# Kernel optimization log

Measured on AMD Instinct MI355X. Metric: run time of the kernel, lower is better.

## Reference

```python
import jax, jax.numpy as jnp
import numpy as np

N = 100000      # nodes
E = 800000      # edges (avg degree 8)
F_IN = 512      # num_features
H = 256         # 2 * embedding_size
D_OUT = 128     # embedding_size


def setup_inputs() -> dict:
    key = jax.random.key(0)
    ks = jax.random.split(key, 5)
    x = jax.random.normal(ks[0], (N, F_IN), dtype=jnp.float32)
    edge_index = jax.random.randint(ks[1], (2, E), 0, N, dtype=jnp.int64)
    W1 = jax.random.normal(ks[2], (F_IN, H), dtype=jnp.float32) * (1.0 / np.sqrt(F_IN))
    b1 = jnp.zeros((H,), dtype=jnp.float32)
    W2 = jax.random.normal(ks[3], (H, D_OUT), dtype=jnp.float32) * (1.0 / np.sqrt(H))
    b2 = jnp.zeros((D_OUT,), dtype=jnp.float32)
    return {"x": x, "edge_index": edge_index, "W1": W1, "b1": b1, "W2": W2, "b2": b2}


def _gcn_conv(x, edge_index, W, b):
    # PyG GCNConv: add self-loops, symmetric deg^-1/2 normalization,
    # linear transform, scatter-add aggregation at destination nodes.
    n = x.shape[0]
    loop = jnp.arange(n, dtype=edge_index.dtype)
    src = jnp.concatenate([edge_index[0], loop])  # source j
    dst = jnp.concatenate([edge_index[1], loop])  # target i
    h = x @ W                                      # [N, F_out]
    deg = jax.ops.segment_sum(jnp.ones_like(dst, dtype=h.dtype), dst, num_segments=n)
    dinv = jnp.where(deg > 0, jax.lax.rsqrt(deg), 0.0)
    norm = dinv[src] * dinv[dst]                   # [E + N]
    msg = h[src] * norm[:, None]                   # gather + scale
    out = jax.ops.segment_sum(msg, dst, num_segments=n)
    return out + b


def reference(x, edge_index, W1, b1, W2, b2):
    h = jax.nn.relu(_gcn_conv(x, edge_index, W1, b1))
    # F.dropout with training=False is identity (eval mode)
    return _gcn_conv(h, edge_index, W2, b2)
```

## Files before the change

kernel.cpp:

```cpp
#include <hip/hip_runtime.h>


typedef float   f32x4  __attribute__((ext_vector_type(4)));
typedef float   f32x2  __attribute__((ext_vector_type(2)));
typedef __bf16  bf16x8 __attribute__((ext_vector_type(8)));
typedef __bf16  bf16x4 __attribute__((ext_vector_type(4)));
typedef __bf16  bf16x2 __attribute__((ext_vector_type(2)));

#define FIN 512
#define HID 256
#define DOUT 128

__device__ __forceinline__ void gload16(const void* g, void* l) {
    __builtin_amdgcn_global_load_lds((const __attribute__((address_space(1))) void*)g,
                                     (__attribute__((address_space(3))) void*)l, 16, 0, 0);
}

__global__ void k_count(const int* __restrict__ dst, int E, int* __restrict__ cnt) {
    int e = blockIdx.x * 256 + threadIdx.x;
    if (e < E) atomicAdd(&cnt[dst[e]], 1);
}

__global__ void k_scan1(const int* __restrict__ cnt, int* __restrict__ off,
                        int* __restrict__ sums, int n) {
    __shared__ int s[1024];
    int i = blockIdx.x * 1024 + threadIdx.x;
    int v = (i < n) ? cnt[i] : 0;
    s[threadIdx.x] = v;
    __syncthreads();
    for (int d = 1; d < 1024; d <<= 1) {
        int t = (threadIdx.x >= d) ? s[threadIdx.x - d] : 0;
        __syncthreads();
        s[threadIdx.x] += t;
        __syncthreads();
    }
    if (i < n) off[i] = s[threadIdx.x] - v;
    if (threadIdx.x == 1023) sums[blockIdx.x] = s[1023];
}

__global__ void k_scan2(int* __restrict__ sums, int nb) {
    __shared__ int s[128];
    int t = threadIdx.x;
    int v = (t < nb) ? sums[t] : 0;
    s[t] = v;
    __syncthreads();
    for (int d = 1; d < 128; d <<= 1) {
        int u = (t >= d) ? s[t - d] : 0;
        __syncthreads();
        s[t] += u;
        __syncthreads();
    }
    if (t < nb) sums[t] = s[t] - v;
}

__global__ void k_scan_fix(int* __restrict__ off, const int* __restrict__ sums,
                           const int* __restrict__ cnt, float* __restrict__ dinv, int n) {
    int i = blockIdx.x * 256 + threadIdx.x;
    if (i < n) {
        off[i] += sums[i >> 10];
        dinv[i] = rsqrtf((float)(cnt[i] + 1));
    }
}

__global__ void k_fill(const int* __restrict__ src, const int* __restrict__ dst, int E,
                       const int* __restrict__ off, int* __restrict__ cur,
                       int* __restrict__ csr) {
    int e = blockIdx.x * 256 + threadIdx.x;
    if (e < E) {
        int d = dst[e];
        int p = atomicAdd(&cur[d], 1);
        csr[off[d] + p] = src[e];
    }
}

__global__ void k_prep_w(const float* __restrict__ W1, const float* __restrict__ W2,
                         __bf16* __restrict__ W1t, __bf16* __restrict__ W2t) {
    int id = blockIdx.x * 256 + threadIdx.x;
    if (id < FIN * HID) {
        int k = id >> 8, n = id & 255;
        W1t[n * FIN + k] = (__bf16)W1[id];
    }
    int id2 = id - FIN * HID;
    if (id2 >= 0 && id2 < HID * DOUT) {
        int k = id2 >> 7, n = id2 & 127;
        W2t[n * HID + k] = (__bf16)W2[id2];
    }
}

__global__ __launch_bounds__(256, 2) void k_gemm1(
    const float* __restrict__ x, const __bf16* __restrict__ Bt,
    const float* __restrict__ dinv, __bf16* __restrict__ g1, int M) {
    __shared__ __bf16 Albuf[2][128 * 32];
    __shared__ __bf16 Blbuf[2][256 * 32];

    const int tid = threadIdx.x;
    const int l = tid & 63, wid = tid >> 6;
    const int wm = wid & 1, wn = wid >> 1;
    const int r15 = l & 15, hi = l >> 4;
    const long bm = blockIdx.x;

    const int arow = tid >> 1, aseg = tid & 1;
    long ag = bm * 128 + arow;
    if (ag >= M) ag = M - 1;
    const float* aptr = x + ag * (long)FIN + aseg * 16;
    const int aoff = arow * 32 + aseg * 16;

    const int bo0 = wid * 4096;

    f32x4 acc[4][8] = {};

    auto stageB = [&](int kb, int buf) {
#pragma unroll
        for (int i = 0; i < 4; ++i) {
            int ob = bo0 + i * 1024;
            int o = ob + l * 16;
            int n = o >> 6, cb = o & 63;
            const char* src = (const char*)Bt + (long)n * (FIN * 2) + kb * 64 + cb;
            gload16(src, (char*)&Blbuf[buf][0] + ob);
        }
    };

    stageB(0, 0);
    {
        const f32x4* p = (const f32x4*)aptr;
        f32x4 p0 = p[0], p1 = p[1], p2 = p[2], p3 = p[3];
        bf16x8 w0, w1;
#pragma unroll
        for (int j = 0; j < 4; ++j) {
            w0[j] = (__bf16)p0[j]; w0[j + 4] = (__bf16)p1[j];
            w1[j] = (__bf16)p2[j]; w1[j + 4] = (__bf16)p3[j];
        }
        *(bf16x8*)&Albuf[0][aoff] = w0;
        *(bf16x8*)&Albuf[0][aoff + 8] = w1;
    }
    __syncthreads();

    int cur = 0;
    constexpr int NT = FIN / 32;
    for (int kb = 0; kb < NT; ++kb) {
        const int nxt = cur ^ 1;
        const bool pf = (kb + 1 < NT);
        f32x4 p0, p1, p2, p3;
        if (pf) {
            stageB(kb + 1, nxt);
            const f32x4* p = (const f32x4*)(aptr + (kb + 1) * 32);
            p0 = p[0]; p1 = p[1]; p2 = p[2]; p3 = p[3];
        }

        bf16x8 af[4], bfr[8];
#pragma unroll
        for (int m = 0; m < 4; ++m)
            af[m] = *(const bf16x8*)&Albuf[cur][(wm * 64 + m * 16 + r15) * 32 + hi * 8];
#pragma unroll
        for (int n = 0; n < 8; ++n)
            bfr[n] = *(const bf16x8*)&Blbuf[cur][(wn * 128 + n * 16 + r15) * 32 + hi * 8];
#pragma unroll
        for (int m = 0; m < 4; ++m)
#pragma unroll
            for (int n = 0; n < 8; ++n)
                acc[m][n] = __builtin_amdgcn_mfma_f32_16x16x32_bf16(bfr[n], af[m], acc[m][n], 0, 0, 0);

        if (pf) {
            bf16x8 w0, w1;
#pragma unroll
            for (int j = 0; j < 4; ++j) {
                w0[j] = (__bf16)p0[j]; w0[j + 4] = (__bf16)p1[j];
                w1[j] = (__bf16)p2[j]; w1[j + 4] = (__bf16)p3[j];
            }
            *(bf16x8*)&Albuf[nxt][aoff] = w0;
            *(bf16x8*)&Albuf[nxt][aoff + 8] = w1;
        }
        __syncthreads();
        cur = nxt;
    }

#pragma unroll
    for (int m = 0; m < 4; ++m) {
        long rg = bm * 128 + wm * 64 + m * 16 + r15;
        if (rg >= M) continue;
        float di = dinv[rg];
#pragma unroll
        for (int n = 0; n < 8; ++n) {
            bf16x4 o;
            o[0] = (__bf16)(acc[m][n][0] * di);
            o[1] = (__bf16)(acc[m][n][1] * di);
            o[2] = (__bf16)(acc[m][n][2] * di);
            o[3] = (__bf16)(acc[m][n][3] * di);
            int c = wn * 128 + n * 16 + hi * 4;
            *(bf16x4*)(g1 + rg * (long)HID + c) = o;
        }
    }
}

__global__ __launch_bounds__(256, 3) void k_gemm2(
    const __bf16* __restrict__ z1, const __bf16* __restrict__ Bt,
    const float* __restrict__ dinv, __bf16* __restrict__ g2, int M) {
    __shared__ __bf16 Albuf[2][128 * 32];
    __shared__ __bf16 Blbuf[2][128 * 32];

    const int tid = threadIdx.x;
    const int l = tid & 63, wid = tid >> 6;
    const int wm = wid & 1, wn = wid >> 1;
    const int r15 = l & 15, hi = l >> 4;
    const long bm = blockIdx.x;

    f32x4 acc[4][4] = {};

    auto stage = [&](int kb, int buf) {
#pragma unroll
        for (int i = 0; i < 2; ++i) {
            int ob = wid * 2048 + i * 1024;
            int o = ob + l * 16;
            long r = bm * 128 + (o >> 6);
            if (r >= M) r = M - 1;
            const char* src = (const char*)z1 + r * (HID * 2) + kb * 64 + (o & 63);
            gload16(src, (char*)&Albuf[buf][0] + ob);
        }
#pragma unroll
        for (int i = 0; i < 2; ++i) {
            int ob = wid * 2048 + i * 1024;
            int o = ob + l * 16;
            int n = o >> 6;
            const char* src = (const char*)Bt + (long)n * (HID * 2) + kb * 64 + (o & 63);
            gload16(src, (char*)&Blbuf[buf][0] + ob);
        }
    };

    stage(0, 0);
    __syncthreads();

    int cur = 0;
    constexpr int NT = HID / 32;
    for (int kb = 0; kb < NT; ++kb) {
        const int nxt = cur ^ 1;
        if (kb + 1 < NT) stage(kb + 1, nxt);

        bf16x8 af[4], bfr[4];
#pragma unroll
        for (int m = 0; m < 4; ++m)
            af[m] = *(const bf16x8*)&Albuf[cur][(wm * 64 + m * 16 + r15) * 32 + hi * 8];
#pragma unroll
        for (int n = 0; n < 4; ++n)
            bfr[n] = *(const bf16x8*)&Blbuf[cur][(wn * 64 + n * 16 + r15) * 32 + hi * 8];
#pragma unroll
        for (int m = 0; m < 4; ++m)
#pragma unroll
            for (int n = 0; n < 4; ++n)
                acc[m][n] = __builtin_amdgcn_mfma_f32_16x16x32_bf16(bfr[n], af[m], acc[m][n], 0, 0, 0);

        __syncthreads();
        cur = nxt;
    }

#pragma unroll
    for (int m = 0; m < 4; ++m) {
        long rg = bm * 128 + wm * 64 + m * 16 + r15;
        if (rg >= M) continue;
        float di = dinv[rg];
#pragma unroll
        for (int n = 0; n < 4; ++n) {
            bf16x4 o;
            o[0] = (__bf16)(acc[m][n][0] * di);
            o[1] = (__bf16)(acc[m][n][1] * di);
            o[2] = (__bf16)(acc[m][n][2] * di);
            o[3] = (__bf16)(acc[m][n][3] * di);
            int c = wn * 64 + n * 16 + hi * 4;
            *(bf16x4*)(g2 + rg * (long)DOUT + c) = o;
        }
    }
}

__global__ void k_agg1(const __bf16* __restrict__ g1, const int* __restrict__ csr,
                       const int* __restrict__ off, const int* __restrict__ cnt,
                       const float* __restrict__ dinv, const float* __restrict__ b1,
                       __bf16* __restrict__ z1, int n) {
    int node = blockIdx.x * 4 + (threadIdx.x >> 6);
    if (node >= n) return;
    int l = threadIdx.x & 63;
    const __bf16* base = g1 + (size_t)l * 4;
    bf16x4 v = *(const bf16x4*)(base + (size_t)node * HID);
    float a0 = (float)v[0], a1 = (float)v[1], a2 = (float)v[2], a3 = (float)v[3];
    float c0 = 0.f, c1 = 0.f, c2 = 0.f, c3 = 0.f;
    int e = off[node], e0 = e + cnt[node];
    for (; e + 3 < e0; e += 4) {
        int sA = csr[e], sB = csr[e + 1], sC = csr[e + 2], sD = csr[e + 3];
        bf16x4 uA = *(const bf16x4*)(base + (size_t)sA * HID);
        bf16x4 uB = *(const bf16x4*)(base + (size_t)sB * HID);
        bf16x4 uC = *(const bf16x4*)(base + (size_t)sC * HID);
        bf16x4 uD = *(const bf16x4*)(base + (size_t)sD * HID);
        a0 += (float)uA[0] + (float)uC[0]; c0 += (float)uB[0] + (float)uD[0];
        a1 += (float)uA[1] + (float)uC[1]; c1 += (float)uB[1] + (float)uD[1];
        a2 += (float)uA[2] + (float)uC[2]; c2 += (float)uB[2] + (float)uD[2];
        a3 += (float)uA[3] + (float)uC[3]; c3 += (float)uB[3] + (float)uD[3];
    }
    for (; e < e0; ++e) {
        int s = csr[e];
        bf16x4 u = *(const bf16x4*)(base + (size_t)s * HID);
        a0 += (float)u[0]; a1 += (float)u[1]; a2 += (float)u[2]; a3 += (float)u[3];
    }
    float di = dinv[node];
    f32x4 b = *(const f32x4*)(b1 + l * 4);
    bf16x4 o;
    o[0] = (__bf16)fmaxf((a0 + c0) * di + b[0], 0.f);
    o[1] = (__bf16)fmaxf((a1 + c1) * di + b[1], 0.f);
    o[2] = (__bf16)fmaxf((a2 + c2) * di + b[2], 0.f);
    o[3] = (__bf16)fmaxf((a3 + c3) * di + b[3], 0.f);
    *(bf16x4*)(z1 + (size_t)node * HID + l * 4) = o;
}

__global__ void k_agg2(const __bf16* __restrict__ g2, const int* __restrict__ csr,
                       const int* __restrict__ off, const int* __restrict__ cnt,
                       const float* __restrict__ dinv, const float* __restrict__ b2,
                       float* __restrict__ out, int n) {
    int node = blockIdx.x * 4 + (threadIdx.x >> 6);
    if (node >= n) return;
    int l = threadIdx.x & 63;
    const __bf16* base = g2 + (size_t)l * 2;
    bf16x2 v = *(const bf16x2*)(base + (size_t)node * DOUT);
    float a0 = (float)v[0], a1 = (float)v[1];
    float c0 = 0.f, c1 = 0.f;
    int e = off[node], e0 = e + cnt[node];
    for (; e + 3 < e0; e += 4) {
        int sA = csr[e], sB = csr[e + 1], sC = csr[e + 2], sD = csr[e + 3];
        bf16x2 uA = *(const bf16x2*)(base + (size_t)sA * DOUT);
        bf16x2 uB = *(const bf16x2*)(base + (size_t)sB * DOUT);
        bf16x2 uC = *(const bf16x2*)(base + (size_t)sC * DOUT);
        bf16x2 uD = *(const bf16x2*)(base + (size_t)sD * DOUT);
        a0 += (float)uA[0] + (float)uC[0]; c0 += (float)uB[0] + (float)uD[0];
        a1 += (float)uA[1] + (float)uC[1]; c1 += (float)uB[1] + (float)uD[1];
    }
    for (; e < e0; ++e) {
        int s = csr[e];
        bf16x2 u = *(const bf16x2*)(base + (size_t)s * DOUT);
        a0 += (float)u[0]; a1 += (float)u[1];
    }
    float di = dinv[node];
    f32x2 b = *(const f32x2*)(b2 + l * 2);
    f32x2 o;
    o[0] = (a0 + c0) * di + b[0];
    o[1] = (a1 + c1) * di + b[1];
    *(f32x2*)(out + (size_t)node * DOUT + l * 2) = o;
}

extern "C" void kernel_launch(void* const* d_in, const int* in_sizes, int n_in,
                              void* d_out, int out_size, void* d_ws, size_t ws_size,
                              hipStream_t stream) {
    const float* x  = (const float*)d_in[0];
    const int*   ei = (const int*)d_in[1];
    const float* W1 = (const float*)d_in[2];
    const float* b1 = (const float*)d_in[3];
    const float* W2 = (const float*)d_in[4];
    const float* b2 = (const float*)d_in[5];
    float* out = (float*)d_out;

    const int N = in_sizes[0] / FIN;
    const int E = in_sizes[1] / 2;
    const int* srcA = ei;
    const int* dstA = ei + E;

    uint8_t* w = (uint8_t*)d_ws;
    auto take = [&](size_t bytes) { uint8_t* p = w; w += (bytes + 255) & ~(size_t)255; return p; };
    int*    cnt  = (int*)take((size_t)N * 4);
    int*    cur  = (int*)take((size_t)N * 4);
    int*    off  = (int*)take((size_t)N * 4);
    float*  dinv = (float*)take((size_t)N * 4);
    int*    sums = (int*)take(4096);
    int*    csr  = (int*)take((size_t)E * 4);
    __bf16* W1t  = (__bf16*)take((size_t)FIN * HID * 2);
    __bf16* W2t  = (__bf16*)take((size_t)HID * DOUT * 2);
    __bf16* g1   = (__bf16*)take((size_t)N * HID * 2);
    __bf16* z1   = (__bf16*)take((size_t)N * HID * 2);
    __bf16* g2   = (__bf16*)take((size_t)N * DOUT * 2);

    hipMemsetAsync(cnt, 0, (size_t)N * 4, stream);
    hipMemsetAsync(cur, 0, (size_t)N * 4, stream);
    k_count<<<(E + 255) / 256, 256, 0, stream>>>(dstA, E, cnt);
    int nb = (N + 1023) / 1024;
    k_scan1<<<nb, 1024, 0, stream>>>(cnt, off, sums, N);
    k_scan2<<<1, 128, 0, stream>>>(sums, nb);
    k_scan_fix<<<(N + 255) / 256, 256, 0, stream>>>(off, sums, cnt, dinv, N);
    k_fill<<<(E + 255) / 256, 256, 0, stream>>>(srcA, dstA, E, off, cur, csr);

    k_prep_w<<<(FIN * HID + HID * DOUT + 255) / 256, 256, 0, stream>>>(W1, W2, W1t, W2t);

    const int gm = (N + 127) / 128;

    k_gemm1<<<gm, 256, 0, stream>>>(x, W1t, dinv, g1, N);
    k_agg1<<<(N + 3) / 4, 256, 0, stream>>>(g1, csr, off, cnt, dinv, b1, z1, N);
    k_gemm2<<<gm, 256, 0, stream>>>(z1, W2t, dinv, g2, N);
    k_agg2<<<(N + 3) / 4, 256, 0, stream>>>(g2, csr, off, cnt, dinv, b2, out, N);
}
```

Measured before the change: 564.9 us.

## Widen aggregation gathers to half-wave per node and merge prep launches

The aggregation kernels now give each node 32 lanes instead of 64. Each lane loads 16-byte (layer 1) or 8-byte (layer 2) vectors, and the unroll is deeper at 8 edges per iteration, so more gather loads are in flight. The weight conversion is folded into the degree-count kernel, and the two memsets become one contiguous memset. This cuts launch overhead and raises memory-level parallelism in the gather-bound aggregation, at the cost of more registers per thread.

```diff
diff --git a/kernel.cpp b/kernel.cpp
--- a/kernel.cpp
+++ b/kernel.cpp
@@ -2,10 +2,8 @@
 
 
 typedef float   f32x4  __attribute__((ext_vector_type(4)));
-typedef float   f32x2  __attribute__((ext_vector_type(2)));
 typedef __bf16  bf16x8 __attribute__((ext_vector_type(8)));
 typedef __bf16  bf16x4 __attribute__((ext_vector_type(4)));
-typedef __bf16  bf16x2 __attribute__((ext_vector_type(2)));
 
 #define FIN 512
 #define HID 256
@@ -16,9 +14,25 @@
                                      (__attribute__((address_space(3))) void*)l, 16, 0, 0);
 }
 
-__global__ void k_count(const int* __restrict__ dst, int E, int* __restrict__ cnt) {
-    int e = blockIdx.x * 256 + threadIdx.x;
-    if (e < E) atomicAdd(&cnt[dst[e]], 1);
+__global__ void k_count_prep(const int* __restrict__ dst, int E, int* __restrict__ cnt,
+                             const float* __restrict__ W1, const float* __restrict__ W2,
+                             __bf16* __restrict__ W1t, __bf16* __restrict__ W2t,
+                             int nCountBlk) {
+    if (blockIdx.x < nCountBlk) {
+        int e = blockIdx.x * 256 + threadIdx.x;
+        if (e < E) atomicAdd(&cnt[dst[e]], 1);
+    } else {
+        int id = (blockIdx.x - nCountBlk) * 256 + threadIdx.x;
+        if (id < FIN * HID) {
+            int k = id >> 8, n = id & 255;
+            W1t[n * FIN + k] = (__bf16)W1[id];
+        }
+        int id2 = id - FIN * HID;
+        if (id2 >= 0 && id2 < HID * DOUT) {
+            int k = id2 >> 7, n = id2 & 127;
+            W2t[n * HID + k] = (__bf16)W2[id2];
+        }
+    }
 }
 
 __global__ void k_scan1(const int* __restrict__ cnt, int* __restrict__ off,
@@ -70,20 +84,6 @@
         int d = dst[e];
         int p = atomicAdd(&cur[d], 1);
         csr[off[d] + p] = src[e];
-    }
-}
-
-__global__ void k_prep_w(const float* __restrict__ W1, const float* __restrict__ W2,
-                         __bf16* __restrict__ W1t, __bf16* __restrict__ W2t) {
-    int id = blockIdx.x * 256 + threadIdx.x;
-    if (id < FIN * HID) {
-        int k = id >> 8, n = id & 255;
-        W1t[n * FIN + k] = (__bf16)W1[id];
-    }
-    int id2 = id - FIN * HID;
-    if (id2 >= 0 && id2 < HID * DOUT) {
-        int k = id2 >> 7, n = id2 & 127;
-        W2t[n * HID + k] = (__bf16)W2[id2];
     }
 }
 
@@ -274,72 +274,120 @@
                        const int* __restrict__ off, const int* __restrict__ cnt,
                        const float* __restrict__ dinv, const float* __restrict__ b1,
                        __bf16* __restrict__ z1, int n) {
-    int node = blockIdx.x * 4 + (threadIdx.x >> 6);
+    int node = blockIdx.x * 8 + (threadIdx.x >> 5);
     if (node >= n) return;
-    int l = threadIdx.x & 63;
-    const __bf16* base = g1 + (size_t)l * 4;
-    bf16x4 v = *(const bf16x4*)(base + (size_t)node * HID);
-    float a0 = (float)v[0], a1 = (float)v[1], a2 = (float)v[2], a3 = (float)v[3];
-    float c0 = 0.f, c1 = 0.f, c2 = 0.f, c3 = 0.f;
+    int l = threadIdx.x & 31;
+    const __bf16* base = g1 + (size_t)l * 8;
+    float a[8], c[8];
+    {
+        bf16x8 v = *(const bf16x8*)(base + (size_t)node * HID);
+#pragma unroll
+        for (int j = 0; j < 8; ++j) { a[j] = (float)v[j]; c[j] = 0.f; }
+    }
     int e = off[node], e0 = e + cnt[node];
+    for (; e + 7 < e0; e += 8) {
+        int s0 = csr[e], s1 = csr[e + 1], s2 = csr[e + 2], s3 = csr[e + 3];
+        int s4 = csr[e + 4], s5 = csr[e + 5], s6 = csr[e + 6], s7 = csr[e + 7];
+        bf16x8 u0 = *(const bf16x8*)(base + (size_t)s0 * HID);
+        bf16x8 u1 = *(const bf16x8*)(base + (size_t)s1 * HID);
+        bf16x8 u2 = *(const bf16x8*)(base + (size_t)s2 * HID);
+        bf16x8 u3 = *(const bf16x8*)(base + (size_t)s3 * HID);
+        bf16x8 u4 = *(const bf16x8*)(base + (size_t)s4 * HID);
+        bf16x8 u5 = *(const bf16x8*)(base + (size_t)s5 * HID);
+        bf16x8 u6 = *(const bf16x8*)(base + (size_t)s6 * HID);
+        bf16x8 u7 = *(const bf16x8*)(base + (size_t)s7 * HID);
+#pragma unroll
+        for (int j = 0; j < 8; ++j) {
+            a[j] += (float)u0[j] + (float)u2[j] + (float)u4[j] + (float)u6[j];
+            c[j] += (float)u1[j] + (float)u3[j] + (float)u5[j] + (float)u7[j];
+        }
+    }
     for (; e + 3 < e0; e += 4) {
-        int sA = csr[e], sB = csr[e + 1], sC = csr[e + 2], sD = csr[e + 3];
-        bf16x4 uA = *(const bf16x4*)(base + (size_t)sA * HID);
-        bf16x4 uB = *(const bf16x4*)(base + (size_t)sB * HID);
-        bf16x4 uC = *(const bf16x4*)(base + (size_t)sC * HID);
-        bf16x4 uD = *(const bf16x4*)(base + (size_t)sD * HID);
-        a0 += (float)uA[0] + (float)uC[0]; c0 += (float)uB[0] + (float)uD[0];
-        a1 += (float)uA[1] + (float)uC[1]; c1 += (float)uB[1] + (float)uD[1];
-        a2 += (float)uA[2] + (float)uC[2]; c2 += (float)uB[2] + (float)uD[2];
-        a3 += (float)uA[3] + (float)uC[3]; c3 += (float)uB[3] + (float)uD[3];
+        int s0 = csr[e], s1 = csr[e + 1], s2 = csr[e + 2], s3 = csr[e + 3];
+        bf16x8 u0 = *(const bf16x8*)(base + (size_t)s0 * HID);
+        bf16x8 u1 = *(const bf16x8*)(base + (size_t)s1 * HID);
+        bf16x8 u2 = *(const bf16x8*)(base + (size_t)s2 * HID);
+        bf16x8 u3 = *(const bf16x8*)(base + (size_t)s3 * HID);
+#pragma unroll
+        for (int j = 0; j < 8; ++j) {
+            a[j] += (float)u0[j] + (float)u2[j];
+            c[j] += (float)u1[j] + (float)u3[j];
+        }
     }
     for (; e < e0; ++e) {
         int s = csr[e];
-        bf16x4 u = *(const bf16x4*)(base + (size_t)s * HID);
-        a0 += (float)u[0]; a1 += (float)u[1]; a2 += (float)u[2]; a3 += (float)u[3];
+        bf16x8 u = *(const bf16x8*)(base + (size_t)s * HID);
+#pragma unroll
+        for (int j = 0; j < 8; ++j) a[j] += (float)u[j];
     }
     float di = dinv[node];
-    f32x4 b = *(const f32x4*)(b1 + l * 4);
-    bf16x4 o;
-    o[0] = (__bf16)fmaxf((a0 + c0) * di + b[0], 0.f);
-    o[1] = (__bf16)fmaxf((a1 + c1) * di + b[1], 0.f);
-    o[2] = (__bf16)fmaxf((a2 + c2) * di + b[2], 0.f);
-    o[3] = (__bf16)fmaxf((a3 + c3) * di + b[3], 0.f);
-    *(bf16x4*)(z1 + (size_t)node * HID + l * 4) = o;
+    f32x4 bA = *(const f32x4*)(b1 + l * 8);
+    f32x4 bB = *(const f32x4*)(b1 + l * 8 + 4);
+    bf16x8 o;
+#pragma unroll
+    for (int j = 0; j < 4; ++j) {
+        o[j]     = (__bf16)fmaxf((a[j] + c[j]) * di + bA[j], 0.f);
+        o[j + 4] = (__bf16)fmaxf((a[j + 4] + c[j + 4]) * di + bB[j], 0.f);
+    }
+    *(bf16x8*)(z1 + (size_t)node * HID + l * 8) = o;
 }
 
 __global__ void k_agg2(const __bf16* __restrict__ g2, const int* __restrict__ csr,
                        const int* __restrict__ off, const int* __restrict__ cnt,
                        const float* __restrict__ dinv, const float* __restrict__ b2,
                        float* __restrict__ out, int n) {
-    int node = blockIdx.x * 4 + (threadIdx.x >> 6);
+    int node = blockIdx.x * 8 + (threadIdx.x >> 5);
     if (node >= n) return;
-    int l = threadIdx.x & 63;
-    const __bf16* base = g2 + (size_t)l * 2;
-    bf16x2 v = *(const bf16x2*)(base + (size_t)node * DOUT);
-    float a0 = (float)v[0], a1 = (float)v[1];
-    float c0 = 0.f, c1 = 0.f;
+    int l = threadIdx.x & 31;
+    const __bf16* base = g2 + (size_t)l * 4;
+    float a[4], c[4];
+    {
+        bf16x4 v = *(const bf16x4*)(base + (size_t)node * DOUT);
+#pragma unroll
+        for (int j = 0; j < 4; ++j) { a[j] = (float)v[j]; c[j] = 0.f; }
+    }
     int e = off[node], e0 = e + cnt[node];
+    for (; e + 7 < e0; e += 8) {
+        int s0 = csr[e], s1 = csr[e + 1], s2 = csr[e + 2], s3 = csr[e + 3];
+        int s4 = csr[e + 4], s5 = csr[e + 5], s6 = csr[e + 6], s7 = csr[e + 7];
+        bf16x4 u0 = *(const bf16x4*)(base + (size_t)s0 * DOUT);
+        bf16x4 u1 = *(const bf16x4*)(base + (size_t)s1 * DOUT);
+        bf16x4 u2 = *(const bf16x4*)(base + (size_t)s2 * DOUT);
+        bf16x4 u3 = *(const bf16x4*)(base + (size_t)s3 * DOUT);
+        bf16x4 u4 = *(const bf16x4*)(base + (size_t)s4 * DOUT);
+        bf16x4 u5 = *(const bf16x4*)(base + (size_t)s5 * DOUT);
+        bf16x4 u6 = *(const bf16x4*)(base + (size_t)s6 * DOUT);
+        bf16x4 u7 = *(const bf16x4*)(base + (size_t)s7 * DOUT);
+#pragma unroll
+        for (int j = 0; j < 4; ++j) {
+            a[j] += (float)u0[j] + (float)u2[j] + (float)u4[j] + (float)u6[j];
+            c[j] += (float)u1[j] + (float)u3[j] + (float)u5[j] + (float)u7[j];
+        }
+    }
     for (; e + 3 < e0; e += 4) {
-        int sA = csr[e], sB = csr[e + 1], sC = csr[e + 2], sD = csr[e + 3];
-        bf16x2 uA = *(const bf16x2*)(base + (size_t)sA * DOUT);
-        bf16x2 uB = *(const bf16x2*)(base + (size_t)sB * DOUT);
-        bf16x2 uC = *(const bf16x2*)(base + (size_t)sC * DOUT);
-        bf16x2 uD = *(const bf16x2*)(base + (size_t)sD * DOUT);
-        a0 += (float)uA[0] + (float)uC[0]; c0 += (float)uB[0] + (float)uD[0];
-        a1 += (float)uA[1] + (float)uC[1]; c1 += (float)uB[1] + (float)uD[1];
+        int s0 = csr[e], s1 = csr[e + 1], s2 = csr[e + 2], s3 = csr[e + 3];
+        bf16x4 u0 = *(const bf16x4*)(base + (size_t)s0 * DOUT);
+        bf16x4 u1 = *(const bf16x4*)(base + (size_t)s1 * DOUT);
+        bf16x4 u2 = *(const bf16x4*)(base + (size_t)s2 * DOUT);
+        bf16x4 u3 = *(const bf16x4*)(base + (size_t)s3 * DOUT);
+#pragma unroll
+        for (int j = 0; j < 4; ++j) {
+            a[j] += (float)u0[j] + (float)u2[j];
+            c[j] += (float)u1[j] + (float)u3[j];
+        }
     }
     for (; e < e0; ++e) {
         int s = csr[e];
-        bf16x2 u = *(const bf16x2*)(base + (size_t)s * DOUT);
-        a0 += (float)u[0]; a1 += (float)u[1];
+        bf16x4 u = *(const bf16x4*)(base + (size_t)s * DOUT);
+#pragma unroll
+        for (int j = 0; j < 4; ++j) a[j] += (float)u[j];
     }
     float di = dinv[node];
-    f32x2 b = *(const f32x2*)(b2 + l * 2);
-    f32x2 o;
-    o[0] = (a0 + c0) * di + b[0];
-    o[1] = (a1 + c1) * di + b[1];
-    *(f32x2*)(out + (size_t)node * DOUT + l * 2) = o;
+    f32x4 b = *(const f32x4*)(b2 + l * 4);
+    f32x4 o;
+#pragma unroll
+    for (int j = 0; j < 4; ++j) o[j] = (a[j] + c[j]) * di + b[j];
+    *(f32x4*)(out + (size_t)node * DOUT + l * 4) = o;
 }
 
 extern "C" void kernel_launch(void* const* d_in, const int* in_sizes, int n_in,
@@ -372,21 +420,22 @@
     __bf16* z1   = (__bf16*)take((size_t)N * HID * 2);
     __bf16* g2   = (__bf16*)take((size_t)N * DOUT * 2);
 
-    hipMemsetAsync(cnt, 0, (size_t)N * 4, stream);
-    hipMemsetAsync(cur, 0, (size_t)N * 4, stream);
-    k_count<<<(E + 255) / 256, 256, 0, stream>>>(dstA, E, cnt);
+    hipMemsetAsync(cnt, 0, (size_t)((uint8_t*)off - (uint8_t*)cnt), stream);
+
+    const int nCountBlk = (E + 255) / 256;
+    const int nPrepBlk = (FIN * HID + HID * DOUT + 255) / 256;
+    k_count_prep<<<nCountBlk + nPrepBlk, 256, 0, stream>>>(dstA, E, cnt, W1, W2, W1t, W2t, nCountBlk);
+
     int nb = (N + 1023) / 1024;
     k_scan1<<<nb, 1024, 0, stream>>>(cnt, off, sums, N);
     k_scan2<<<1, 128, 0, stream>>>(sums, nb);
     k_scan_fix<<<(N + 255) / 256, 256, 0, stream>>>(off, sums, cnt, dinv, N);
     k_fill<<<(E + 255) / 256, 256, 0, stream>>>(srcA, dstA, E, off, cur, csr);
 
-    k_prep_w<<<(FIN * HID + HID * DOUT + 255) / 256, 256, 0, stream>>>(W1, W2, W1t, W2t);
-
     const int gm = (N + 127) / 128;
 
     k_gemm1<<<gm, 256, 0, stream>>>(x, W1t, dinv, g1, N);
-    k_agg1<<<(N + 3) / 4, 256, 0, stream>>>(g1, csr, off, cnt, dinv, b1, z1, N);
+    k_agg1<<<(N + 7) / 8, 256, 0, stream>>>(g1, csr, off, cnt, dinv, b1, z1, N);
     k_gemm2<<<gm, 256, 0, stream>>>(z1, W2t, dinv, g2, N);
-    k_agg2<<<(N + 3) / 4, 256, 0, stream>>>(g2, csr, off, cnt, dinv, b2, out, N);
-}
+    k_agg2<<<(N + 7) / 8, 256, 0, stream>>>(g2, csr, off, cnt, dinv, b2, out, N);
+}
```

Measured after the change: 547.4 us. -3.1%, faster.
